# Performance work log

Hardware: AMD Instinct MI355X
Metric: run time of the kernel (lower is better)

The kernel has to match this reference:

```python
import jax, jax.numpy as jnp
import numpy as np


def setup_inputs() -> dict:
    key = jax.random.key(0)
    ks = jax.random.split(key, 9)
    B, C, H, W = 8, 256, 64, 64
    Co = 256
    s = 1.0 / np.sqrt(C)
    return {
        "x": jax.random.normal(ks[0], (B, C, H, W), dtype=jnp.float32),
        "wq": jax.random.normal(ks[1], (Co, C), dtype=jnp.float32) * s,
        "bq": jnp.zeros((Co,), dtype=jnp.float32),
        "wk": jax.random.normal(ks[2], (Co, C), dtype=jnp.float32) * s,
        "bk": jnp.zeros((Co,), dtype=jnp.float32),
        "wv": jax.random.normal(ks[3], (Co, C), dtype=jnp.float32) * s,
        "bv": jnp.zeros((Co,), dtype=jnp.float32),
        "wo": jax.random.normal(ks[4], (C, Co), dtype=jnp.float32) * s,
        "bo": jnp.zeros((C,), dtype=jnp.float32),
    }


def reference(x, wq, bq, wk, bk, wv, bv, wo, bo):
    B, C, H, W = x.shape
    # 1x1 conv == per-pixel matmul. Flatten spatial dims: [B, N, C], N = H*W
    xf = x.reshape(B, C, H * W).transpose(0, 2, 1)  # [B, N, C]
    q = jnp.einsum("bnc,oc->bno", xf, wq) + bq      # [B, N, Co]
    k = jnp.einsum("bnc,oc->bno", xf, wk) + bk      # [B, N, Co]
    v = jnp.einsum("bnc,oc->bno", xf, wv) + bv      # [B, N, Co]
    # attention[b, i, j] = q[b, i] . k[b, j]  (no scaling, matches source)
    attn = jax.nn.softmax(jnp.einsum("bio,bjo->bij", q, k), axis=-1)  # [B, N, N]
    # out[b, i, c] = sum_j attn[b, i, j] * v[b, j, c]
    out = jnp.einsum("bij,bjo->bio", attn, v)       # [B, N, Co]
    out = jnp.einsum("bno,co->bnc", out, wo) + bo   # [B, N, C]
    return out.transpose(0, 2, 1).reshape(B, C, H, W)
```

## Files before the change

kernel.cpp:

```cpp
#include <hip/hip_runtime.h>
#include <hip/hip_fp16.h>

typedef _Float16 f16;
typedef _Float16 f16x4 __attribute__((ext_vector_type(4)));
typedef _Float16 f16x8 __attribute__((ext_vector_type(8)));
typedef float f32x4 __attribute__((ext_vector_type(4)));
typedef float f32x16 __attribute__((ext_vector_type(16)));

static constexpr int CB = 8;
static constexpr int CC = 256;
static constexpr int CN = 4096;
static constexpr float LOG2E = 1.44269504088896f;

#define MFMA(a, b, c)   __builtin_amdgcn_mfma_f32_16x16x32_f16((a), (b), (c), 0, 0, 0)
#define MFMA32(a, b, c) __builtin_amdgcn_mfma_f32_32x32x16_f16((a), (b), (c), 0, 0, 0)

__device__ __forceinline__ void gll16(const void* g, void* l) {
  __builtin_amdgcn_global_load_lds(
      (const __attribute__((address_space(1))) unsigned int*)g,
      (__attribute__((address_space(3))) unsigned int*)l, 16, 0, 0);
}

__global__ __launch_bounds__(256) void prep_weights(const float* __restrict__ wq,
    const float* __restrict__ wk, const float* __restrict__ wv,
    const float* __restrict__ wo, f16* __restrict__ W) {
  int i = blockIdx.x * 256 + threadIdx.x;
  W[i]          = (f16)wq[i];
  W[65536 + i]  = (f16)wk[i];
  W[131072 + i] = (f16)wv[i];
  W[196608 + i] = (f16)wo[i];
}

__global__ __launch_bounds__(256) void qkv_kernel(const float* __restrict__ x,
    const f16* __restrict__ Wq, const f16* __restrict__ Wk, const f16* __restrict__ Wv,
    const float* __restrict__ bq, const float* __restrict__ bk, const float* __restrict__ bv,
    f16* __restrict__ Q, f16* __restrict__ K, f16* __restrict__ Vt) {
  __shared__ f16 xf[64][264];
  const int b  = blockIdx.x >> 6;
  const int n0 = (blockIdx.x & 63) << 6;
  const int t  = threadIdx.x;
  const float* xb = x + (size_t)b * CC * CN;
  {
    int c = t >> 4;
    const int nn = (t & 15) << 2;
    #pragma unroll
    for (int pass = 0; pass < 16; ++pass, c += 16) {
      const float4 v = *(const float4*)(xb + (size_t)c * CN + n0 + nn);
      xf[nn + 0][c] = (f16)v.x;
      xf[nn + 1][c] = (f16)v.y;
      xf[nn + 2][c] = (f16)v.z;
      xf[nn + 3][c] = (f16)v.w;
    }
  }
  __syncthreads();
  const int w = t >> 6, l = t & 63, lr = l & 15, lh = l >> 4;

  f16x8 xff[8];
  #pragma unroll
  for (int kk = 0; kk < 8; ++kk)
    xff[kk] = *(const f16x8*)&xf[w * 16 + lr][kk * 32 + lh * 8];

  const size_t qkrow = ((size_t)b * CN + n0 + w * 16 + lr) * CC;

  #pragma unroll 1
  for (int mat = 0; mat < 2; ++mat) {
    const f16* W = mat ? Wk : Wq;
    const float* bias = mat ? bk : bq;
    f16* dst = mat ? K : Q;
    f32x4 acc[16];
    #pragma unroll
    for (int m = 0; m < 16; ++m) acc[m] = f32x4{0.f, 0.f, 0.f, 0.f};
    #pragma unroll
    for (int kk = 0; kk < 8; ++kk) {
      #pragma unroll
      for (int m = 0; m < 16; ++m) {
        f16x8 af = *(const f16x8*)&W[(size_t)(m * 16 + lr) * CC + kk * 32 + lh * 8];
        acc[m] = MFMA(af, xff[kk], acc[m]);
      }
    }
    #pragma unroll
    for (int m = 0; m < 16; ++m) {
      const int o = m * 16 + lh * 4;
      const float4 bs = *(const float4*)&bias[o];
      f16x4 hv;
      hv[0] = (f16)(acc[m][0] + bs.x);
      hv[1] = (f16)(acc[m][1] + bs.y);
      hv[2] = (f16)(acc[m][2] + bs.z);
      hv[3] = (f16)(acc[m][3] + bs.w);
      *(f16x4*)&dst[qkrow + o] = hv;
    }
  }
  {
    f32x4 acc[16];
    #pragma unroll
    for (int m = 0; m < 16; ++m) acc[m] = f32x4{0.f, 0.f, 0.f, 0.f};
    #pragma unroll
    for (int kk = 0; kk < 8; ++kk) {
      #pragma unroll
      for (int m = 0; m < 16; ++m) {
        f16x8 bf = *(const f16x8*)&Wv[(size_t)(m * 16 + lr) * CC + kk * 32 + lh * 8];
        acc[m] = MFMA(xff[kk], bf, acc[m]);
      }
    }
    #pragma unroll
    for (int m = 0; m < 16; ++m) {
      const int o = m * 16 + lr;
      const float bvs = bv[o];
      f16x4 hv;
      #pragma unroll
      for (int j = 0; j < 4; ++j) hv[j] = (f16)(acc[m][j] + bvs);
      *(f16x4*)&Vt[((size_t)b * CC + o) * CN + n0 + w * 16 + lh * 4] = hv;
    }
  }
}

__global__ __launch_bounds__(512, 2) void attn_kernel(const f16* __restrict__ Q,
    const f16* __restrict__ K, const f16* __restrict__ Vt, f16* __restrict__ O) {
  __shared__ __align__(16) char SMEM[89088];

  const int bid = blockIdx.x;
  const int lb = ((bid & 7) << 5) | (bid >> 3);
  const int b  = lb >> 5;
  const int q0 = (lb & 31) << 7;
  const int t  = threadIdx.x;
  const int w  = t >> 6, l = t & 63, ln = l & 31, lh = l >> 5;
  const int g  = w >> 1, hv = w & 1;

  const f16* Qb = Q  + (size_t)b * CN * CC;
  const f16* Kb = K  + (size_t)b * CN * CC;
  const f16* Vb = Vt + (size_t)b * CC * CN;

  float* const ALf = (float*)(SMEM + 88064 + w * 128);
  char*  const PB  = SMEM + 65536 + w * 2816;

  auto stage = [&](int buf, int kv0) {
    char* base = SMEM + (buf << 15);
    if (w < 4) {
      const f16* src = Kb + (size_t)(kv0 + ln) * CC + (w * 4) * 16 + 8 * lh;
      #pragma unroll
      for (int j = 0; j < 4; ++j)
        gll16(src + j * 16, base + ((w * 4 + j) << 10));
    } else {
      const int j0 = (w - 4) * 4;
      #pragma unroll
      for (int p = 0; p < 2; ++p) {
        const f16* src = Vb + (size_t)(((j0 >> 1) + p) * 32 + ln) * CN + kv0 + 8 * lh;
        gll16(src,      base + ((16 + j0 + 2 * p)     << 10));
        gll16(src + 16, base + ((16 + j0 + 2 * p + 1) << 10));
      }
    }
  };

  const int qrow = q0 + 32 * g + ln;
  f16x8 qf[16];
  #pragma unroll
  for (int ks = 0; ks < 16; ++ks)
    qf[ks] = *(const f16x8*)(Qb + (size_t)qrow * CC + ks * 16 + 8 * lh);

  f32x16 oacc[4];
  #pragma unroll
  for (int ot = 0; ot < 4; ++ot)
    #pragma unroll
    for (int i = 0; i < 16; ++i) oacc[ot][i] = 0.0f;
  float mrun = -3e38f, lrun = 0.0f;

  stage(0, 0);
  __syncthreads();

  for (int it = 0; it < 128; ++it) {
    const int cur = it & 1;
    if (it < 127) stage(cur ^ 1, (it + 1) * 32);

    f32x16 s;
    #pragma unroll
    for (int i = 0; i < 16; ++i) s[i] = 0.0f;
    #pragma unroll
    for (int ks = 0; ks < 16; ++ks) {
      const f16x8 kf = *(const f16x8*)(SMEM + (cur << 15) + (ks << 10) + l * 16);
      s = MFMA32(kf, qf[ks], s);
    }

    float pmax = -3e38f;
    #pragma unroll
    for (int r = 0; r < 16; ++r) pmax = fmaxf(pmax, s[r]);
    pmax = fmaxf(pmax, __shfl_xor(pmax, 32));
    const bool need = !__all(pmax - mrun <= 8.0f);
    float mnew = mrun;
    if (need) mnew = fmaxf(mrun, pmax);
    float psum = 0.0f;
    f16 pc[16];
    #pragma unroll
    for (int r = 0; r < 16; ++r) {
      const float p = exp2f((s[r] - mnew) * LOG2E);
      psum += p;
      pc[r] = (f16)p;
    }
    psum += __shfl_xor(psum, 32);
    if (need) {
      const float alpha = exp2f((mrun - mnew) * LOG2E);
      lrun = lrun * alpha + psum;
      mrun = mnew;
      if (l < 32) ALf[ln] = alpha;
      #pragma unroll
      for (int r = 0; r < 16; ++r) {
        const float fr = ALf[(r & 3) + 8 * (r >> 2) + 4 * lh];
        #pragma unroll
        for (int ot = 0; ot < 4; ++ot) oacc[ot][r] *= fr;
      }
    } else {
      lrun += psum;
    }

    #pragma unroll
    for (int rg = 0; rg < 4; ++rg) {
      f16x4 pv = { pc[4 * rg], pc[4 * rg + 1], pc[4 * rg + 2], pc[4 * rg + 3] };
      *(f16x4*)(PB + 88 * ln + 16 * rg + 8 * lh) = pv;
    }
    const f16x8 pa0 = *(const f16x8*)(PB + 88 * ln + 16 * lh);
    const f16x8 pa1 = *(const f16x8*)(PB + 88 * ln + 32 + 16 * lh);

    #pragma unroll
    for (int ot = 0; ot < 4; ++ot) {
      const int f0 = 16 + 8 * hv + 2 * ot;
      const f16x8 v0 = *(const f16x8*)(SMEM + (cur << 15) + (f0 << 10) + l * 16);
      oacc[ot] = MFMA32(pa0, v0, oacc[ot]);
      const f16x8 v1 = *(const f16x8*)(SMEM + (cur << 15) + ((f0 + 1) << 10) + l * 16);
      oacc[ot] = MFMA32(pa1, v1, oacc[ot]);
    }
    __syncthreads();
  }

  if (l < 32) ALf[ln] = 1.0f / lrun;
  f16* Ob = O + ((size_t)b * CN + q0 + 32 * g) * CC + 128 * hv;
  #pragma unroll
  for (int r = 0; r < 16; ++r) {
    const int q = (r & 3) + 8 * (r >> 2) + 4 * lh;
    const float inv = ALf[q];
    #pragma unroll
    for (int ot = 0; ot < 4; ++ot)
      Ob[(size_t)q * CC + ot * 32 + ln] = (f16)(oacc[ot][r] * inv);
  }
}

__global__ __launch_bounds__(256) void oproj_kernel(const f16* __restrict__ O,
    const f16* __restrict__ Wo, const float* __restrict__ bo, float* __restrict__ out) {
  const int b  = blockIdx.x >> 6;
  const int n0 = (blockIdx.x & 63) << 6;
  const int t  = threadIdx.x;
  const int w = t >> 6, l = t & 63, lr = l & 15, lh = l >> 4;
  const f16* orow = O + ((size_t)b * CN + n0 + w * 16 + lr) * CC;
  f32x4 acc[16];
  #pragma unroll
  for (int m = 0; m < 16; ++m) acc[m] = f32x4{0.f, 0.f, 0.f, 0.f};
  #pragma unroll
  for (int kk = 0; kk < 8; ++kk) {
    const f16x8 bf = *(const f16x8*)&orow[kk * 32 + lh * 8];
    #pragma unroll
    for (int m = 0; m < 16; ++m) {
      f16x8 af = *(const f16x8*)&Wo[(size_t)(m * 16 + lr) * CC + kk * 32 + lh * 8];
      acc[m] = MFMA(af, bf, acc[m]);
    }
  }
  #pragma unroll
  for (int m = 0; m < 16; ++m) {
    const int c = m * 16 + lh * 4;
    const float4 bv4 = *(const float4*)&bo[c];
    const size_t base = ((size_t)b * CC + c) * CN + n0 + w * 16 + lr;
    out[base + 0 * (size_t)CN] = acc[m][0] + bv4.x;
    out[base + 1 * (size_t)CN] = acc[m][1] + bv4.y;
    out[base + 2 * (size_t)CN] = acc[m][2] + bv4.z;
    out[base + 3 * (size_t)CN] = acc[m][3] + bv4.w;
  }
}

extern "C" void kernel_launch(void* const* d_in, const int* in_sizes, int n_in,
                              void* d_out, int out_size, void* d_ws, size_t ws_size,
                              hipStream_t stream) {
  const float* x  = (const float*)d_in[0];
  const float* wq = (const float*)d_in[1];
  const float* bq = (const float*)d_in[2];
  const float* wk = (const float*)d_in[3];
  const float* bk = (const float*)d_in[4];
  const float* wv = (const float*)d_in[5];
  const float* bv = (const float*)d_in[6];
  const float* wo = (const float*)d_in[7];
  const float* bo = (const float*)d_in[8];

  f16* W  = (f16*)d_ws;
  f16* Qd = W + 262144;
  f16* Kd = Qd + (size_t)CB * CN * CC;
  f16* Vt = Kd + (size_t)CB * CN * CC;
  f16* Od = Vt + (size_t)CB * CN * CC;

  prep_weights<<<256, 256, 0, stream>>>(wq, wk, wv, wo, W);
  qkv_kernel<<<512, 256, 0, stream>>>(x, W, W + 65536, W + 131072, bq, bk, bv, Qd, Kd, Vt);
  attn_kernel<<<256, 512, 0, stream>>>(Qd, Kd, Vt, Od);
  oproj_kernel<<<512, 256, 0, stream>>>(Od, W + 196608, bo, (float*)d_out);
}
```

Measured before the change: 396.6 us.

## Shrink attention blocks to 4 waves and repack P via permlane swaps

Halves the attention block from 8 to 4 waves (64 query rows per block) and doubles the grid, so each wave now stages both K and V tiles, and LDS use drops enough for more blocks per CU. The softmax probabilities are no longer round-tripped through a per-wave LDS buffer to reach the MFMA A-operand layout. Instead they are packed to f16 pairs and rearranged across lane halves with v_permlane32_swap. This removes LDS writes and reads plus the associated latency. In exchange, K/V tiles are loaded twice as often per query row, which doubles L2/global traffic for K and V.

```diff
diff --git a/kernel.cpp b/kernel.cpp
--- a/kernel.cpp
+++ b/kernel.cpp
@@ -6,6 +6,8 @@
 typedef _Float16 f16x8 __attribute__((ext_vector_type(8)));
 typedef float f32x4 __attribute__((ext_vector_type(4)));
 typedef float f32x16 __attribute__((ext_vector_type(16)));
+typedef unsigned int u32;
+typedef u32 u32x4 __attribute__((ext_vector_type(4)));
 
 static constexpr int CB = 8;
 static constexpr int CC = 256;
@@ -19,6 +21,15 @@
   __builtin_amdgcn_global_load_lds(
       (const __attribute__((address_space(1))) unsigned int*)g,
       (__attribute__((address_space(3))) unsigned int*)l, 16, 0, 0);
+}
+
+__device__ __forceinline__ void plswap(u32& a, u32& b) {
+  asm volatile("v_permlane32_swap_b32 %0, %1" : "+v"(a), "+v"(b));
+}
+
+__device__ __forceinline__ u32 pk(float lo, float hi) {
+  auto h = __builtin_amdgcn_cvt_pkrtz(lo, hi);
+  return __builtin_bit_cast(u32, h);
 }
 
 __global__ __launch_bounds__(256) void prep_weights(const float* __restrict__ wq,
@@ -114,14 +125,14 @@
   }
 }
 
-__global__ __launch_bounds__(512, 2) void attn_kernel(const f16* __restrict__ Q,
+__global__ __launch_bounds__(256, 2) void attn_kernel(const f16* __restrict__ Q,
     const f16* __restrict__ K, const f16* __restrict__ Vt, f16* __restrict__ O) {
-  __shared__ __align__(16) char SMEM[89088];
+  __shared__ __align__(16) char SMEM[66048];
 
   const int bid = blockIdx.x;
-  const int lb = ((bid & 7) << 5) | (bid >> 3);
-  const int b  = lb >> 5;
-  const int q0 = (lb & 31) << 7;
+  const int lb = ((bid & 7) << 6) | (bid >> 3);
+  const int b  = lb >> 6;
+  const int q0 = (lb & 63) << 6;
   const int t  = threadIdx.x;
   const int w  = t >> 6, l = t & 63, ln = l & 31, lh = l >> 5;
   const int g  = w >> 1, hv = w & 1;
@@ -130,24 +141,20 @@
   const f16* Kb = K  + (size_t)b * CN * CC;
   const f16* Vb = Vt + (size_t)b * CC * CN;
 
-  float* const ALf = (float*)(SMEM + 88064 + w * 128);
-  char*  const PB  = SMEM + 65536 + w * 2816;
+  float* const ALf = (float*)(SMEM + 65536 + w * 128);
 
   auto stage = [&](int buf, int kv0) {
     char* base = SMEM + (buf << 15);
-    if (w < 4) {
-      const f16* src = Kb + (size_t)(kv0 + ln) * CC + (w * 4) * 16 + 8 * lh;
-      #pragma unroll
-      for (int j = 0; j < 4; ++j)
-        gll16(src + j * 16, base + ((w * 4 + j) << 10));
-    } else {
-      const int j0 = (w - 4) * 4;
-      #pragma unroll
-      for (int p = 0; p < 2; ++p) {
-        const f16* src = Vb + (size_t)(((j0 >> 1) + p) * 32 + ln) * CN + kv0 + 8 * lh;
-        gll16(src,      base + ((16 + j0 + 2 * p)     << 10));
-        gll16(src + 16, base + ((16 + j0 + 2 * p + 1) << 10));
-      }
+    const f16* ksrc = Kb + (size_t)(kv0 + ln) * CC + (w * 4) * 16 + 8 * lh;
+    #pragma unroll
+    for (int j = 0; j < 4; ++j)
+      gll16(ksrc + j * 16, base + ((w * 4 + j) << 10));
+    #pragma unroll
+    for (int p = 0; p < 2; ++p) {
+      const int f = w * 4 + 2 * p;
+      const f16* vsrc = Vb + (size_t)((f >> 1) * 32 + ln) * CN + kv0 + 8 * lh;
+      gll16(vsrc,      base + ((16 + f)     << 10));
+      gll16(vsrc + 16, base + ((16 + f + 1) << 10));
     }
   };
 
@@ -188,12 +195,11 @@
     float mnew = mrun;
     if (need) mnew = fmaxf(mrun, pmax);
     float psum = 0.0f;
-    f16 pc[16];
+    float p[16];
     #pragma unroll
     for (int r = 0; r < 16; ++r) {
-      const float p = exp2f((s[r] - mnew) * LOG2E);
-      psum += p;
-      pc[r] = (f16)p;
+      p[r] = exp2f((s[r] - mnew) * LOG2E);
+      psum += p[r];
     }
     psum += __shfl_xor(psum, 32);
     if (need) {
@@ -211,13 +217,13 @@
       lrun += psum;
     }
 
-    #pragma unroll
-    for (int rg = 0; rg < 4; ++rg) {
-      f16x4 pv = { pc[4 * rg], pc[4 * rg + 1], pc[4 * rg + 2], pc[4 * rg + 3] };
-      *(f16x4*)(PB + 88 * ln + 16 * rg + 8 * lh) = pv;
-    }
-    const f16x8 pa0 = *(const f16x8*)(PB + 88 * ln + 16 * lh);
-    const f16x8 pa1 = *(const f16x8*)(PB + 88 * ln + 32 + 16 * lh);
+    u32 pw[8];
+    #pragma unroll
+    for (int i = 0; i < 8; ++i) pw[i] = pk(p[2 * i], p[2 * i + 1]);
+    plswap(pw[0], pw[2]); plswap(pw[1], pw[3]);
+    plswap(pw[4], pw[6]); plswap(pw[5], pw[7]);
+    const f16x8 pa0 = __builtin_bit_cast(f16x8, u32x4{pw[0], pw[1], pw[2], pw[3]});
+    const f16x8 pa1 = __builtin_bit_cast(f16x8, u32x4{pw[4], pw[5], pw[6], pw[7]});
 
     #pragma unroll
     for (int ot = 0; ot < 4; ++ot) {
@@ -294,6 +300,6 @@
 
   prep_weights<<<256, 256, 0, stream>>>(wq, wk, wv, wo, W);
   qkv_kernel<<<512, 256, 0, stream>>>(x, W, W + 65536, W + 131072, bq, bk, bv, Qd, Kd, Vt);
-  attn_kernel<<<256, 512, 0, stream>>>(Qd, Kd, Vt, Od);
+  attn_kernel<<<512, 256, 0, stream>>>(Qd, Kd, Vt, Od);
   oproj_kernel<<<512, 256, 0, stream>>>(Od, W + 196608, bo, (float*)d_out);
 }
```

After: 417.9 us. 1.05x slower.
